# Performance work log

Hardware: AMD Instinct MI355X
Metric: run time of the kernel (lower is better)

## Reference

```python
import jax, jax.numpy as jnp
import numpy as np

N = 4096      # number of nodes (len(batch_node))
K = 8         # number of adjacency channels
C = 256       # in_channels == out_channels
E = 131072    # number of edges (avg degree 32)


def setup_inputs() -> dict:
    key = jax.random.key(0)
    k1, k2, k3 = jax.random.split(key, 3)
    h = jax.random.normal(k1, (C, N), dtype=jnp.float32)
    X = jax.random.normal(k2, (E, K), dtype=jnp.float32)
    # sample unique (src, dst) pairs so the scatter-set has no duplicate writes
    rng = np.random.default_rng(0)
    flat = rng.choice(N * N, size=E, replace=False)
    edge_index = jnp.asarray(np.stack([flat // N, flat % N]).astype(np.int32))
    batch_node = jnp.zeros((N,), dtype=jnp.float32)
    # glorot uniform: stdv = sqrt(6 / (in + out))
    stdv = np.sqrt(6.0 / (C + C)).astype(np.float32)
    weight = jax.random.uniform(k3, (K, C, C), dtype=jnp.float32,
                                minval=-stdv, maxval=stdv)
    bias = jnp.zeros((C,), dtype=jnp.float32)
    return {"h": h, "X": X, "edge_index": edge_index,
            "batch_node": batch_node, "weight": weight, "bias": bias}


def reference(h, X, edge_index, batch_node, weight, bias):
    Kk = weight.shape[0]
    Nn = batch_node.shape[0]
    # scatter edge features into K dense [N, N] adjacency tensors
    resx = jnp.zeros((Kk, Nn, Nn), dtype=h.dtype)
    resx = resx.at[:, edge_index[0], edge_index[1]].set(X.T)
    # res[k] = h @ resx[k] : [K, C, N]
    res = jnp.einsum('cn,knm->kcm', h, resx)
    # sum_k weight[k] @ res[k] : [C, N]  (in_channels == out_channels)
    out = jnp.einsum('kio,kon->in', weight, res)
    # (res.T + bias).T == res + bias[:, None]
    return out + bias[:, None]
```

## Files before the change

### kernel.cpp

```cpp
#include <hip/hip_runtime.h>

constexpr int NN = 4096;
constexpr int KC = 8;
constexpr int CC = 256;
constexpr int NE = 131072;
constexpr int KK = KC * CC;
constexpr int CAP = 96;

typedef short bf16x8 __attribute__((ext_vector_type(8)));
typedef float f32x4 __attribute__((ext_vector_type(4)));

__device__ inline unsigned short f2bf(float f) {
    union { float f; unsigned int u; } v; v.f = f;
    unsigned int u = v.u;
    u += 0x7fffu + ((u >> 16) & 1u);
    return (unsigned short)(u >> 16);
}
__device__ inline float bf2f(unsigned short u) {
    union { unsigned int i; float f; } w; w.i = ((unsigned int)u) << 16; return w.f;
}

__global__ __launch_bounds__(256) void k_prep(
    const float* __restrict__ h, const float* __restrict__ w,
    unsigned short* __restrict__ ht, unsigned short* __restrict__ A,
    int* __restrict__ cursor) {
    int b = blockIdx.x;
    int t = threadIdx.x;
    if (b < 1024) {
        __shared__ float tile[32][33];
        int nb = b >> 3, cb = b & 7;
        int n0 = nb * 32, c0 = cb * 32;
        int tx = t & 31, ty = t >> 5;
#pragma unroll
        for (int j = 0; j < 32; j += 8)
            tile[ty + j][tx] = h[(size_t)(c0 + ty + j) * NN + n0 + tx];
        __syncthreads();
#pragma unroll
        for (int j = 0; j < 32; j += 8)
            ht[(size_t)(n0 + ty + j) * CC + c0 + tx] = f2bf(tile[tx][ty + j]);
    } else {
        int idx = (b - 1024) * 256 + t;
        if (idx < NN) cursor[idx] = 0;
        int o = idx & 255;
        int k = (idx >> 8) & 7;
        int i = idx >> 11;
        A[idx] = f2bf(w[(k << 16) | (i << 8) | o]);
    }
}

__global__ void k_fill(const int* __restrict__ edge_src, const int* __restrict__ edge_dst,
                       int* __restrict__ cursor, int2* __restrict__ bins) {
    int e = blockIdx.x * 256 + threadIdx.x;
    int d = edge_dst[e];
    int slot = atomicAdd(&cursor[d], 1);
    if (slot < CAP) bins[d * CAP + slot] = make_int2(e, edge_src[e]);
}

__device__ inline void agg_accum(f32x4 acc[KC], float4 v, float4 xa, float4 xb) {
    f32x4 vv = {v.x, v.y, v.z, v.w};
    acc[0] += xa.x * vv; acc[1] += xa.y * vv;
    acc[2] += xa.z * vv; acc[3] += xa.w * vv;
    acc[4] += xb.x * vv; acc[5] += xb.y * vv;
    acc[6] += xb.z * vv; acc[7] += xb.w * vv;
}

__global__ __launch_bounds__(256) void k_agg(
    const int* __restrict__ cursor, const int2* __restrict__ bins,
    const float* __restrict__ X, const unsigned short* __restrict__ ht,
    unsigned short* __restrict__ agg) {
    const int wid  = __builtin_amdgcn_readfirstlane(threadIdx.x >> 6);
    const int lane = threadIdx.x & 63;
    const int n = blockIdx.x * 4 + wid;
    int cnt = cursor[n];
    cnt = cnt > CAP ? CAP : cnt;
    const int p0 = n * CAP;
    const int p1 = p0 + cnt;
    const float4* X4 = reinterpret_cast<const float4*>(X);

    f32x4 acc[KC] = {};

    int p = p0;
    for (; p + 8 <= p1; p += 8) {
        int2 q[8];
        ushort4 u[8];
#pragma unroll
        for (int j = 0; j < 8; ++j) q[j] = bins[p + j];
#pragma unroll
        for (int j = 0; j < 8; ++j)
            u[j] = *(const ushort4*)(ht + (size_t)q[j].y * CC + 4 * lane);
#pragma unroll
        for (int j = 0; j < 8; ++j) {
            float4 v = {bf2f(u[j].x), bf2f(u[j].y), bf2f(u[j].z), bf2f(u[j].w)};
            agg_accum(acc, v, X4[q[j].x * 2], X4[q[j].x * 2 + 1]);
        }
    }
    for (; p < p1; ++p) {
        int2 q = bins[p];
        ushort4 u = *(const ushort4*)(ht + (size_t)q.y * CC + 4 * lane);
        float4 v = {bf2f(u.x), bf2f(u.y), bf2f(u.z), bf2f(u.w)};
        agg_accum(acc, v, X4[q.x * 2], X4[q.x * 2 + 1]);
    }

    unsigned short* op = agg + (size_t)n * KK + 4 * lane;
#pragma unroll
    for (int k = 0; k < KC; ++k) {
        ushort4 w;
        w.x = f2bf(acc[k][0]); w.y = f2bf(acc[k][1]);
        w.z = f2bf(acc[k][2]); w.w = f2bf(acc[k][3]);
        *reinterpret_cast<ushort4*>(op + k * CC) = w;
    }
}

__global__ __launch_bounds__(256) void k_gemm_mfma(
    const unsigned short* __restrict__ A, const unsigned short* __restrict__ B,
    const float* __restrict__ bias, float* __restrict__ out) {
    constexpr int BM = 64, BN = 32, BK = 64;
    constexpr int NT = KK / BK;
    __shared__ unsigned short As[2][BM][BK];
    __shared__ unsigned short Bs[2][BN][BK];
    const int tid  = threadIdx.x;
    const int wid  = tid >> 6;
    const int lane = tid & 63;

    const int raw = blockIdx.x;
    const int swz = (raw & 7) * 64 + (raw >> 3);
    const int i0 = (swz & 3) * BM;
    const int n0 = (swz >> 2) * BN;

    const int wm = (wid & 1) * 32;
    const int wn = (wid >> 1) * 16;

    const int lrow = lane >> 3;
    const int csrc = ((lane & 7) ^ lrow) * 8;

    f32x4 acc[2] = {};

#define STAGE(T, BUF)                                                              \
    do {                                                                           \
        int kc0_ = (T) * BK;                                                       \
        _Pragma("unroll")                                                          \
        for (int q = 0; q < 2; ++q) {                                              \
            int seg = wid + q * 4;                                                 \
            int row = seg * 8 + lrow;                                              \
            __builtin_amdgcn_global_load_lds(                                      \
                (const __attribute__((address_space(1))) void*)(                   \
                    A + (size_t)(i0 + row) * KK + kc0_ + csrc),                    \
                (__attribute__((address_space(3))) void*)(                         \
                    (char*)&As[BUF][0][0] + seg * 1024), 16, 0, 0);                \
        }                                                                          \
        {                                                                          \
            int row = wid * 8 + lrow;                                              \
            __builtin_amdgcn_global_load_lds(                                      \
                (const __attribute__((address_space(1))) void*)(                   \
                    B + (size_t)(n0 + row) * KK + kc0_ + csrc),                    \
                (__attribute__((address_space(3))) void*)(                         \
                    (char*)&Bs[BUF][0][0] + wid * 1024), 16, 0, 0);                \
        }                                                                          \
    } while (0)

    STAGE(0, 0);

    const int rA = wm + (lane & 15);
    const int rB = wn + (lane & 15);
    const int sw = lane & 7;
    const int chb = lane >> 4;

    for (int t = 0; t < NT; ++t) {
        int b = t & 1;
        if (t + 1 < NT) {
            STAGE(t + 1, b ^ 1);
            asm volatile("s_waitcnt vmcnt(3)" ::: "memory");
        } else {
            asm volatile("s_waitcnt vmcnt(0)" ::: "memory");
        }
        __builtin_amdgcn_s_barrier();
        asm volatile("" ::: "memory");

        const char* Ab = (const char*)&As[b][0][0];
        const char* Bb = (const char*)&Bs[b][0][0];
#pragma unroll
        for (int ks = 0; ks < BK; ks += 32) {
            const int ch = (ks >> 3) + chb;
            bf16x8 a0 = *(const bf16x8*)(Ab + rA * 128 + ((ch ^ sw) << 4));
            bf16x8 a1 = *(const bf16x8*)(Ab + (rA + 16) * 128 + ((ch ^ sw) << 4));
            bf16x8 b0 = *(const bf16x8*)(Bb + rB * 128 + ((ch ^ sw) << 4));
            acc[0] = __builtin_amdgcn_mfma_f32_16x16x32_bf16(a0, b0, acc[0], 0, 0, 0);
            acc[1] = __builtin_amdgcn_mfma_f32_16x16x32_bf16(a1, b0, acc[1], 0, 0, 0);
        }
        asm volatile("" ::: "memory");
        __builtin_amdgcn_s_barrier();
    }
#undef STAGE

    const int lr = (lane >> 4) * 4;
    const int lc = lane & 15;
#pragma unroll
    for (int mi = 0; mi < 2; ++mi) {
#pragma unroll
        for (int r = 0; r < 4; ++r) {
            int i = i0 + wm + mi * 16 + lr + r;
            out[(size_t)i * NN + n0 + wn + lc] = acc[mi][r] + bias[i];
        }
    }
}

extern "C" void kernel_launch(void* const* d_in, const int* in_sizes, int n_in,
                              void* d_out, int out_size, void* d_ws, size_t ws_size,
                              hipStream_t stream) {
    const float* h      = (const float*)d_in[0];
    const float* X      = (const float*)d_in[1];
    const int* edge_idx = (const int*)d_in[2];
    const float* weight = (const float*)d_in[4];
    const float* bias   = (const float*)d_in[5];
    float* out = (float*)d_out;

    const int* edge_src = edge_idx;
    const int* edge_dst = edge_idx + NE;

    char* ws = (char*)d_ws;
    unsigned short* ht   = (unsigned short*)(ws);
    unsigned short* Abf  = (unsigned short*)(ws + (2 << 20));
    unsigned short* agg  = (unsigned short*)(ws + (4 << 20));
    size_t meta = (size_t)(20 << 20);
    int* cursor = (int*)(ws + meta);
    int2* bins  = (int2*)(ws + meta + 65536);

    k_prep<<<3072, 256, 0, stream>>>(h, weight, ht, Abf, cursor);
    k_fill<<<NE / 256, 256, 0, stream>>>(edge_src, edge_dst, cursor, bins);
    k_agg<<<NN / 4, 256, 0, stream>>>(cursor, bins, X, ht, agg);
    k_gemm_mfma<<<512, 256, 0, stream>>>(Abf, agg, bias, out);
}
```

Baseline: 54.28 us.

## Merge prep and fill kernels, split node aggregation across two waves

Edge binning, the h transpose and the weight bf16 conversion now run as branches of one kernel, and the cursor is zeroed by a memset beforehand. The change removes a launch and lets binning overlap with the conversion work. The weight conversion is vectorised to four elements per thread. Aggregation now gives each node two waves that each process half of its edges, then combines the halves through shared memory, which doubles the wave count and shortens each wave's serial chain at the cost of a block barrier and an extra LDS reduction.

```diff
diff --git a/kernel.cpp b/kernel.cpp
--- a/kernel.cpp
+++ b/kernel.cpp
@@ -20,16 +20,22 @@
     union { unsigned int i; float f; } w; w.i = ((unsigned int)u) << 16; return w.f;
 }
 
-__global__ __launch_bounds__(256) void k_prep(
+__global__ __launch_bounds__(256) void k_mega(
     const float* __restrict__ h, const float* __restrict__ w,
+    const int* __restrict__ edge_src, const int* __restrict__ edge_dst,
     unsigned short* __restrict__ ht, unsigned short* __restrict__ A,
-    int* __restrict__ cursor) {
+    int* __restrict__ cursor, int2* __restrict__ bins) {
+    __shared__ float tile[32][33];
     int b = blockIdx.x;
     int t = threadIdx.x;
-    if (b < 1024) {
-        __shared__ float tile[32][33];
-        int nb = b >> 3, cb = b & 7;
-        int n0 = nb * 32, c0 = cb * 32;
+    if (b < 512) {
+        int e = b * 256 + t;
+        int d = edge_dst[e];
+        int slot = atomicAdd(&cursor[d], 1);
+        if (slot < CAP) bins[d * CAP + slot] = make_int2(e, edge_src[e]);
+    } else if (b < 1536) {
+        int tt = b - 512;
+        int n0 = (tt >> 3) * 32, c0 = (tt & 7) * 32;
         int tx = t & 31, ty = t >> 5;
 #pragma unroll
         for (int j = 0; j < 32; j += 8)
@@ -39,21 +45,14 @@
         for (int j = 0; j < 32; j += 8)
             ht[(size_t)(n0 + ty + j) * CC + c0 + tx] = f2bf(tile[tx][ty + j]);
     } else {
-        int idx = (b - 1024) * 256 + t;
-        if (idx < NN) cursor[idx] = 0;
-        int o = idx & 255;
-        int k = (idx >> 8) & 7;
-        int i = idx >> 11;
-        A[idx] = f2bf(w[(k << 16) | (i << 8) | o]);
-    }
-}
-
-__global__ void k_fill(const int* __restrict__ edge_src, const int* __restrict__ edge_dst,
-                       int* __restrict__ cursor, int2* __restrict__ bins) {
-    int e = blockIdx.x * 256 + threadIdx.x;
-    int d = edge_dst[e];
-    int slot = atomicAdd(&cursor[d], 1);
-    if (slot < CAP) bins[d * CAP + slot] = make_int2(e, edge_src[e]);
+        int g = (b - 1536) * 256 + t;
+        int idx = g * 4;
+        int o = idx & 255, k = (idx >> 8) & 7, i = idx >> 11;
+        float4 wv = *reinterpret_cast<const float4*>(w + ((k << 16) | (i << 8) | o));
+        ushort4 av;
+        av.x = f2bf(wv.x); av.y = f2bf(wv.y); av.z = f2bf(wv.z); av.w = f2bf(wv.w);
+        *reinterpret_cast<ushort4*>(A + idx) = av;
+    }
 }
 
 __device__ inline void agg_accum(f32x4 acc[KC], float4 v, float4 xa, float4 xb) {
@@ -68,19 +67,23 @@
     const int* __restrict__ cursor, const int2* __restrict__ bins,
     const float* __restrict__ X, const unsigned short* __restrict__ ht,
     unsigned short* __restrict__ agg) {
+    __shared__ f32x4 part[2][KC][64];
     const int wid  = __builtin_amdgcn_readfirstlane(threadIdx.x >> 6);
     const int lane = threadIdx.x & 63;
-    const int n = blockIdx.x * 4 + wid;
+    const int m    = wid >> 1;
+    const int half = wid & 1;
+    const int n = blockIdx.x * 2 + m;
     int cnt = cursor[n];
     cnt = cnt > CAP ? CAP : cnt;
-    const int p0 = n * CAP;
-    const int p1 = p0 + cnt;
+    const int h0 = (cnt + 1) >> 1;
+    const int ps = n * CAP + (half ? h0 : 0);
+    const int pe = n * CAP + (half ? cnt : h0);
     const float4* X4 = reinterpret_cast<const float4*>(X);
 
     f32x4 acc[KC] = {};
 
-    int p = p0;
-    for (; p + 8 <= p1; p += 8) {
+    int p = ps;
+    for (; p + 8 <= pe; p += 8) {
         int2 q[8];
         ushort4 u[8];
 #pragma unroll
@@ -94,20 +97,28 @@
             agg_accum(acc, v, X4[q[j].x * 2], X4[q[j].x * 2 + 1]);
         }
     }
-    for (; p < p1; ++p) {
+    for (; p < pe; ++p) {
         int2 q = bins[p];
         ushort4 u = *(const ushort4*)(ht + (size_t)q.y * CC + 4 * lane);
         float4 v = {bf2f(u.x), bf2f(u.y), bf2f(u.z), bf2f(u.w)};
         agg_accum(acc, v, X4[q.x * 2], X4[q.x * 2 + 1]);
     }
 
-    unsigned short* op = agg + (size_t)n * KK + 4 * lane;
-#pragma unroll
-    for (int k = 0; k < KC; ++k) {
-        ushort4 w;
-        w.x = f2bf(acc[k][0]); w.y = f2bf(acc[k][1]);
-        w.z = f2bf(acc[k][2]); w.w = f2bf(acc[k][3]);
-        *reinterpret_cast<ushort4*>(op + k * CC) = w;
+    if (half == 1) {
+#pragma unroll
+        for (int k = 0; k < KC; ++k) part[m][k][lane] = acc[k];
+    }
+    __syncthreads();
+    if (half == 0) {
+        unsigned short* op = agg + (size_t)n * KK + 4 * lane;
+#pragma unroll
+        for (int k = 0; k < KC; ++k) {
+            f32x4 s = acc[k] + part[m][k][lane];
+            ushort4 w;
+            w.x = f2bf(s[0]); w.y = f2bf(s[1]);
+            w.z = f2bf(s[2]); w.w = f2bf(s[3]);
+            *reinterpret_cast<ushort4*>(op + k * CC) = w;
+        }
     }
 }
 
@@ -225,8 +236,9 @@
     int* cursor = (int*)(ws + meta);
     int2* bins  = (int2*)(ws + meta + 65536);
 
-    k_prep<<<3072, 256, 0, stream>>>(h, weight, ht, Abf, cursor);
-    k_fill<<<NE / 256, 256, 0, stream>>>(edge_src, edge_dst, cursor, bins);
-    k_agg<<<NN / 4, 256, 0, stream>>>(cursor, bins, X, ht, agg);
+    hipMemsetAsync(cursor, 0, NN * sizeof(int), stream);
+    k_mega<<<2048, 256, 0, stream>>>(h, weight, edge_src, edge_dst, ht, Abf,
+                                     cursor, bins);
+    k_agg<<<NN / 2, 256, 0, stream>>>(cursor, bins, X, ht, agg);
     k_gemm_mfma<<<512, 256, 0, stream>>>(Abf, agg, bias, out);
 }
```

New measurement: 54.01 us (median of 2 runs). About the same (-0.5%).
